# Kernel optimization log

Hardware: AMD Instinct MI355X
Metric: run time of the kernel (lower is better)

Reference implementation:

```python
import jax, jax.numpy as jnp
import numpy as np

B, T, D = 1, 4096, 2048
H = 16
D_NOPE, D_ROPE, D_V = 128, 64, 128
D_QK = D_NOPE + D_ROPE          # 192
KV_RANK = 512
SCALE = D_QK ** -0.5
EPS = 1e-5
ROPE_BASE = 10000.0


def _rope_tables(T, d):
    inv_freq = 1.0 / (ROPE_BASE ** (jnp.arange(0, d, 2, dtype=jnp.float32) / d))
    ang = jnp.arange(T, dtype=jnp.float32)[:, None] * inv_freq[None, :]  # [T, d/2]
    return jnp.cos(ang), jnp.sin(ang)


def _apply_rope(x, cos, sin):
    # x: [..., d]; cos/sin broadcastable to [..., d/2]; interleaved pairs
    x1, x2 = x[..., 0::2], x[..., 1::2]
    out = jnp.stack([x1 * cos - x2 * sin, x1 * sin + x2 * cos], axis=-1)
    return out.reshape(x.shape)


def _layernorm(x, g, b):
    mu = jnp.mean(x, axis=-1, keepdims=True)
    var = jnp.var(x, axis=-1, keepdims=True)
    return (x - mu) * jax.lax.rsqrt(var + EPS) * g + b


def setup_inputs() -> dict:
    key = jax.random.key(0)
    ks = jax.random.split(key, 6)
    s = 0.02
    return {
        "x": jax.random.normal(ks[0], (B, T, D), jnp.float32),
        "wq": jax.random.normal(ks[1], (H * D_QK, D), jnp.float32) * s,
        "wkv_a": jax.random.normal(ks[2], (KV_RANK + D_ROPE, D), jnp.float32) * s,
        "kv_gamma": jnp.ones((KV_RANK,), jnp.float32),
        "kv_beta": jnp.zeros((KV_RANK,), jnp.float32),
        "wkv_b": jax.random.normal(ks[3], (H * (D_NOPE + D_V), KV_RANK), jnp.float32) * s,
        "wo": jax.random.normal(ks[4], (D, H * D_V), jnp.float32) * s,
    }


def reference(x, wq, wkv_a, kv_gamma, kv_beta, wkv_b, wo):
    # Query projection (q_lora_rank == 0 path): [B,T,H,D_QK]
    q = (x @ wq.T).reshape(B, T, H, D_QK)
    q_nope, q_pe = q[..., :D_NOPE], q[..., D_NOPE:]

    # Low-rank KV projection: kv latent [B,T,KV_RANK], shared rope key [B,T,D_ROPE]
    kv_full = x @ wkv_a.T
    kv, k_pe = kv_full[..., :KV_RANK], kv_full[..., KV_RANK:]

    cos, sin = _rope_tables(T, D_ROPE)  # [T, D_ROPE/2]
    q_pe = _apply_rope(q_pe, cos[None, :, None, :], sin[None, :, None, :])
    k_pe = _apply_rope(k_pe, cos[None, :, :], sin[None, :, :])

    # Up-project normalized latent to per-head nope-keys and values
    kv = _layernorm(kv, kv_gamma, kv_beta)
    kvb = (kv @ wkv_b.T).reshape(B, T, H, D_NOPE + D_V)
    k_nope, v = kvb[..., :D_NOPE], kvb[..., D_NOPE:]

    # Scores: nope part per head + rope part with shared k_pe
    scores = (
        jnp.einsum("bshd,bthd->bhst", q_nope, k_nope)
        + jnp.einsum("bshd,btd->bhst", q_pe, k_pe)
    ) * SCALE

    causal = jnp.tril(jnp.ones((T, T), bool))
    scores = jnp.where(causal[None, None], scores, -jnp.inf)
    probs = jax.nn.softmax(scores, axis=-1)

    out = jnp.einsum("bhst,bthd->bshd", probs, v).reshape(B, T, H * D_V)
    return out @ wo.T
```

## Files before the change

### kernel.cpp

```cpp
#include <hip/hip_runtime.h>
#include <hip/hip_bf16.h>

typedef __attribute__((ext_vector_type(8))) short bf16x8;
typedef __attribute__((ext_vector_type(4))) float f32x4;
typedef __attribute__((address_space(3))) unsigned int lds_u32;
typedef __attribute__((address_space(1))) const unsigned int glb_u32;

#define LOG2_10000 13.287712379549449f
#define QSCALE (0.07216878364870323f * 1.4426950408889634f)

static __device__ __forceinline__ unsigned short f2bf(float f) {
  union { float f; unsigned int u; } v; v.f = f;
  unsigned int r = v.u + 0x7FFFu + ((v.u >> 16) & 1u);
  return (unsigned short)(r >> 16);
}
static __device__ __forceinline__ float bf2f(unsigned short h) {
  union { unsigned int u; float f; } v; v.u = ((unsigned int)h) << 16;
  return v.f;
}
static __device__ __forceinline__ f32x4 mfma16(bf16x8 a, bf16x8 b, f32x4 c) {
  return __builtin_amdgcn_mfma_f32_16x16x32_bf16(a, b, c, 0, 0, 0);
}
static __device__ __forceinline__ void gl_lds16(const void* g, void* l) {
  __builtin_amdgcn_global_load_lds((glb_u32*)g, (lds_u32*)l, 16, 0, 0);
}

__global__ __launch_bounds__(256) void cast_bf16(const float* __restrict__ src,
                                                 unsigned short* __restrict__ dst,
                                                 int nsrc, int ndst) {
  int i = (blockIdx.x * 256 + threadIdx.x) * 4;
  if (i >= ndst) return;
  float4 v = make_float4(0.f, 0.f, 0.f, 0.f);
  if (i < nsrc) v = *(const float4*)(src + i);
  uint2 o;
  o.x = (unsigned int)f2bf(v.x) | ((unsigned int)f2bf(v.y) << 16);
  o.y = (unsigned int)f2bf(v.z) | ((unsigned int)f2bf(v.w) << 16);
  *(uint2*)(dst + i) = o;
}

template <bool OUTBF>
__global__ __launch_bounds__(256, 2) void gemm_bf16(const unsigned short* __restrict__ A,
                                                    const unsigned short* __restrict__ Bt,
                                                    void* __restrict__ Cv,
                                                    int M, int N, int K, float alpha) {
  __shared__ unsigned short As[128 * 32];
  __shared__ unsigned short Bs[128 * 32];
  const int tid = threadIdx.x;
  const int w = tid >> 6, lane = tid & 63;
  const int quad = lane >> 4, l15 = lane & 15;
  const int wx = w & 1, wy = w >> 1;
  const int bm = blockIdx.y * 128, bn = blockIdx.x * 128;

  f32x4 acc[4][4];
#pragma unroll
  for (int i = 0; i < 4; ++i)
#pragma unroll
    for (int j = 0; j < 4; ++j) { acc[i][j][0] = 0.f; acc[i][j][1] = 0.f; acc[i][j][2] = 0.f; acc[i][j][3] = 0.f; }

  const int lrow = lane >> 2;
  const int lcol = (lane & 3) * 8;
  const unsigned short* Ag = A + (size_t)(bm + w * 16 + lrow) * K + lcol;
  const unsigned short* Bg = Bt + (size_t)(bn + w * 16 + lrow) * K + lcol;
  unsigned short* AsB = &As[(w * 16) * 32];
  unsigned short* BsB = &Bs[(w * 16) * 32];

  for (int k0 = 0; k0 < K; k0 += 32) {
    __syncthreads();
    gl_lds16(Ag + k0, AsB);
    gl_lds16(Ag + (size_t)64 * K + k0, AsB + 64 * 32);
    gl_lds16(Bg + k0, BsB);
    gl_lds16(Bg + (size_t)64 * K + k0, BsB + 64 * 32);
    __syncthreads();
    bf16x8 aF[4], bF[4];
#pragma unroll
    for (int i = 0; i < 4; ++i)
      aF[i] = *(const bf16x8*)&As[(wy * 64 + i * 16 + l15) * 32 + quad * 8];
#pragma unroll
    for (int j = 0; j < 4; ++j)
      bF[j] = *(const bf16x8*)&Bs[(wx * 64 + j * 16 + l15) * 32 + quad * 8];
#pragma unroll
    for (int i = 0; i < 4; ++i)
#pragma unroll
      for (int j = 0; j < 4; ++j)
        acc[i][j] = mfma16(aF[i], bF[j], acc[i][j]);
  }

#pragma unroll
  for (int i = 0; i < 4; ++i)
#pragma unroll
    for (int r = 0; r < 4; ++r) {
      const size_t row = (size_t)(bm + wy * 64 + i * 16 + quad * 4 + r) * (size_t)N;
#pragma unroll
      for (int j = 0; j < 4; ++j) {
        const int col = bn + wx * 64 + j * 16 + l15;
        if (OUTBF) ((unsigned short*)Cv)[row + col] = f2bf(acc[i][j][r] * alpha);
        else       ((float*)Cv)[row + col] = acc[i][j][r];
      }
    }
}

__global__ __launch_bounds__(256) void rope_q_bf(unsigned short* __restrict__ qh) {
  int idx = blockIdx.x * 256 + threadIdx.x;
  int j = idx & 31;
  int th = idx >> 5;
  int h = th & 15;
  int t = th >> 4;
  float fr = exp2f(-(float)j * (LOG2_10000 / 32.f));
  float ang = (float)t * fr;
  float sn, cs;
  sincosf(ang, &sn, &cs);
  unsigned short* p = qh + (size_t)t * 3072 + h * 192 + 128 + 2 * j;
  unsigned int v = *(unsigned int*)p;
  float a = bf2f((unsigned short)v), b = bf2f((unsigned short)(v >> 16));
  float na = a * cs - b * sn, nb = a * sn + b * cs;
  *(unsigned int*)p = (unsigned int)f2bf(na) | ((unsigned int)f2bf(nb) << 16);
}

__global__ __launch_bounds__(256) void ln_rope_k(const float* __restrict__ kvfull,
                                                 const float* __restrict__ gamma,
                                                 const float* __restrict__ beta,
                                                 unsigned short* __restrict__ kvln,
                                                 unsigned short* __restrict__ kpe) {
  const int t = blockIdx.x;
  const int tid = threadIdx.x;
  const float* row = kvfull + (size_t)t * 640;
  float x0 = row[tid], x1 = row[tid + 256];
  float sm = x0 + x1;
  float sq = x0 * x0 + x1 * x1;
#pragma unroll
  for (int off = 1; off < 64; off <<= 1) {
    sm += __shfl_xor(sm, off, 64);
    sq += __shfl_xor(sq, off, 64);
  }
  __shared__ float rs[4], rq[4];
  const int lane = tid & 63, wid = tid >> 6;
  if (lane == 0) { rs[wid] = sm; rq[wid] = sq; }
  __syncthreads();
  float tsm = rs[0] + rs[1] + rs[2] + rs[3];
  float tsq = rq[0] + rq[1] + rq[2] + rq[3];
  float mu = tsm * (1.f / 512.f);
  float var = tsq * (1.f / 512.f) - mu * mu;
  float inv = rsqrtf(var + 1e-5f);
  kvln[(size_t)t * 512 + tid]       = f2bf((x0 - mu) * inv * gamma[tid] + beta[tid]);
  kvln[(size_t)t * 512 + tid + 256] = f2bf((x1 - mu) * inv * gamma[tid + 256] + beta[tid + 256]);
  if (tid < 32) {
    float a = row[512 + 2 * tid], b = row[512 + 2 * tid + 1];
    float fr = exp2f(-(float)tid * (LOG2_10000 / 32.f));
    float ang = (float)t * fr;
    float sn, cs;
    sincosf(ang, &sn, &cs);
    kpe[(size_t)t * 64 + 2 * tid]     = f2bf(a * cs - b * sn);
    kpe[(size_t)t * 64 + 2 * tid + 1] = f2bf(a * sn + b * cs);
  }
}

__global__ __launch_bounds__(256) void transpose_v(const unsigned short* __restrict__ kvb,
                                                   unsigned short* __restrict__ Vt) {
  __shared__ unsigned short tile[64][72];
  const int tb = blockIdx.x * 64;
  const int h  = blockIdx.y >> 1;
  const int c0 = (blockIdx.y & 1) * 64;
  const int tid = threadIdx.x;
  const int r  = tid >> 4;
  const int c4 = (tid & 15) * 4;
#pragma unroll
  for (int rep = 0; rep < 4; ++rep) {
    const int t = rep * 16 + r;
    uint2 d = *(const uint2*)(kvb + (size_t)(tb + t) * 4096 + h * 256 + 128 + c0 + c4);
    *(uint2*)&tile[t][c4] = d;
  }
  __syncthreads();
#pragma unroll
  for (int rep = 0; rep < 4; ++rep) {
    const int c = rep * 16 + r;
    unsigned int lo = (unsigned int)tile[c4 + 0][c] | ((unsigned int)tile[c4 + 1][c] << 16);
    unsigned int hi = (unsigned int)tile[c4 + 2][c] | ((unsigned int)tile[c4 + 3][c] << 16);
    uint2 o; o.x = lo; o.y = hi;
    *(uint2*)(Vt + ((size_t)h * 128 + c0 + c) * 4096 + tb + c4) = o;
  }
}

__global__ __launch_bounds__(256, 2) void attn_mfma(const unsigned short* __restrict__ qh,
                                                    const unsigned short* __restrict__ kvb,
                                                    const unsigned short* __restrict__ kpe,
                                                    const unsigned short* __restrict__ Vt,
                                                    unsigned short* __restrict__ attnh) {
  __shared__ unsigned short sK[6 * 2048];
  __shared__ unsigned short sVt[128 * 64];
  __shared__ unsigned short sP[128 * 72];

  const int bid = blockIdx.x;
  const int h = bid & 15;
  const int z = bid >> 4;
  const int qt = (z < 16) ? (31 - z) : (z - 16);
  const int q0 = qt * 128;
  const int tid = threadIdx.x;
  const int w = tid >> 6, lane = tid & 63;
  const int quad = lane >> 4, l15 = lane & 15;
  const int wq0 = w * 32;

  const unsigned short* kvbh = kvb + h * 256;
  const unsigned short* Vth = Vt + (size_t)h * 128 * 4096;

  bf16x8 qF[2][6];
#pragma unroll
  for (int i = 0; i < 2; ++i)
#pragma unroll
    for (int g = 0; g < 6; ++g) {
      const int grow = q0 + wq0 + i * 16 + l15;
      union { uint4 u; bf16x8 v; } tmp;
      tmp.u = *(const uint4*)(qh + (size_t)grow * 3072 + h * 192 + g * 32 + quad * 8);
      qF[i][g] = tmp.v;
    }

  f32x4 oA[2][8];
  float mi[2], li[2];
#pragma unroll
  for (int i = 0; i < 2; ++i) {
    mi[i] = -1e30f; li[i] = 0.f;
#pragma unroll
    for (int j = 0; j < 8; ++j) { oA[i][j][0] = 0.f; oA[i][j][1] = 0.f; oA[i][j][2] = 0.f; oA[i][j][3] = 0.f; }
  }

  const int nk = 2 * (qt + 1);
  for (int kt = 0; kt < nk; ++kt) {
    const int k0 = kt * 64;
    __syncthreads();

#pragma unroll
    for (int j = 0; j < 6; ++j) {
      const int i = w * 6 + j;
      const int granule = i * 64 + lane;
      const int g = granule >> 8;
      const int key = (granule >> 2) & 63;
      const int col = (g << 5) + ((granule & 3) << 3);
      const unsigned short* src = (col < 128)
          ? kvbh + (size_t)(k0 + key) * 4096 + col
          : kpe + (size_t)(k0 + key) * 64 + (col - 128);
      gl_lds16(src, &sK[i * 512]);
    }
#pragma unroll
    for (int j = 0; j < 4; ++j) {
      const int ii = w * 4 + j;
      const int n = ii * 8 + (lane >> 3);
      const int b = (lane & 7) ^ ((lane >> 3) & 7);
      gl_lds16(Vth + (size_t)n * 4096 + k0 + b * 8, &sVt[ii * 512]);
    }
    __syncthreads();

    f32x4 sc[4][2];
#pragma unroll
    for (int kk = 0; kk < 4; ++kk)
#pragma unroll
      for (int i = 0; i < 2; ++i) { sc[kk][i][0] = 0.f; sc[kk][i][1] = 0.f; sc[kk][i][2] = 0.f; sc[kk][i][3] = 0.f; }
#pragma unroll
    for (int g = 0; g < 6; ++g) {
      bf16x8 kF[4];
#pragma unroll
      for (int kk = 0; kk < 4; ++kk)
        kF[kk] = *(const bf16x8*)&sK[g * 2048 + (kk * 16 + l15) * 32 + quad * 8];
#pragma unroll
      for (int kk = 0; kk < 4; ++kk)
#pragma unroll
        for (int i = 0; i < 2; ++i)
          sc[kk][i] = mfma16(kF[kk], qF[i][g], sc[kk][i]);
    }

    const bool msk = (kt >= 2 * qt);
    float alpha[2];
#pragma unroll
    for (int i = 0; i < 2; ++i) {
      const int grow = q0 + wq0 + i * 16 + l15;
      if (msk) {
#pragma unroll
        for (int kk = 0; kk < 4; ++kk)
#pragma unroll
          for (int rr = 0; rr < 4; ++rr) {
            const int gk = k0 + kk * 16 + quad * 4 + rr;
            if (gk > grow) sc[kk][i][rr] = -1e30f;
          }
      }
      float mx = -1e30f;
#pragma unroll
      for (int kk = 0; kk < 4; ++kk)
#pragma unroll
        for (int rr = 0; rr < 4; ++rr) mx = fmaxf(mx, sc[kk][i][rr]);
      mx = fmaxf(mx, __shfl_xor(mx, 16, 64));
      mx = fmaxf(mx, __shfl_xor(mx, 32, 64));
      const float mnew = fmaxf(mi[i], mx);
      alpha[i] = __builtin_amdgcn_exp2f(mi[i] - mnew);
      float sum = 0.f;
#pragma unroll
      for (int kk = 0; kk < 4; ++kk)
#pragma unroll
        for (int rr = 0; rr < 4; ++rr) {
          const float p = __builtin_amdgcn_exp2f(sc[kk][i][rr] - mnew);
          sc[kk][i][rr] = p;
          sum += p;
        }
      sum += __shfl_xor(sum, 16, 64);
      sum += __shfl_xor(sum, 32, 64);
      li[i] = li[i] * alpha[i] + sum;
      mi[i] = mnew;
    }

#pragma unroll
    for (int i = 0; i < 2; ++i)
#pragma unroll
      for (int rr = 0; rr < 4; ++rr) {
        const float af = __shfl(alpha[i], (lane & 48) | (quad * 4 + rr), 64);
#pragma unroll
        for (int j = 0; j < 8; ++j) oA[i][j][rr] *= af;
      }

#pragma unroll
    for (int kk = 0; kk < 4; ++kk)
#pragma unroll
      for (int i = 0; i < 2; ++i) {
        union { float f; unsigned int u; } p0, p1, p2, p3;
        p0.f = sc[kk][i][0]; p1.f = sc[kk][i][1]; p2.f = sc[kk][i][2]; p3.f = sc[kk][i][3];
        uint2 pk;
        pk.x = (p0.u >> 16) | (p1.u & 0xFFFF0000u);
        pk.y = (p2.u >> 16) | (p3.u & 0xFFFF0000u);
        *(uint2*)&sP[(size_t)(wq0 + i * 16 + l15) * 72 + kk * 16 + quad * 4] = pk;
      }

#pragma unroll
    for (int ks = 0; ks < 2; ++ks) {
      bf16x8 pF[2], vF[8];
#pragma unroll
      for (int i = 0; i < 2; ++i)
        pF[i] = *(const bf16x8*)&sP[(size_t)(wq0 + i * 16 + l15) * 72 + ks * 32 + quad * 8];
#pragma unroll
      for (int j = 0; j < 8; ++j) {
        const int n = j * 16 + l15;
        const int blk = (ks * 4 + quad) ^ (l15 & 7);
        vF[j] = *(const bf16x8*)&sVt[(size_t)n * 64 + blk * 8];
      }
#pragma unroll
      for (int i = 0; i < 2; ++i)
#pragma unroll
        for (int j = 0; j < 8; ++j)
          oA[i][j] = mfma16(pF[i], vF[j], oA[i][j]);
    }
  }

  float linv[2];
  linv[0] = 1.f / li[0];
  linv[1] = 1.f / li[1];
#pragma unroll
  for (int i = 0; i < 2; ++i)
#pragma unroll
    for (int rr = 0; rr < 4; ++rr) {
      const float lf = __shfl(linv[i], (lane & 48) | (quad * 4 + rr), 64);
      const size_t grow = (size_t)(q0 + wq0 + i * 16 + quad * 4 + rr);
#pragma unroll
      for (int j = 0; j < 8; ++j)
        attnh[grow * 2048 + h * 128 + j * 16 + l15] = f2bf(oA[i][j][rr] * lf);
    }
}

extern "C" void kernel_launch(void* const* d_in, const int* in_sizes, int n_in,
                              void* d_out, int out_size, void* d_ws, size_t ws_size,
                              hipStream_t stream) {
  const float* x        = (const float*)d_in[0];
  const float* wq       = (const float*)d_in[1];
  const float* wkv_a    = (const float*)d_in[2];
  const float* kv_gamma = (const float*)d_in[3];
  const float* kv_beta  = (const float*)d_in[4];
  const float* wkv_b    = (const float*)d_in[5];
  const float* wo       = (const float*)d_in[6];
  float* out = (float*)d_out;

  char* p = (char*)d_ws;
  unsigned short* xh    = (unsigned short*)p; p += (size_t)4096 * 2048 * 2;
  unsigned short* wqh   = (unsigned short*)p; p += (size_t)3072 * 2048 * 2;
  unsigned short* wah   = (unsigned short*)p; p += (size_t)640 * 2048 * 2;
  unsigned short* wbh   = (unsigned short*)p; p += (size_t)4096 * 512 * 2;
  unsigned short* woh   = (unsigned short*)p; p += (size_t)2048 * 2048 * 2;
  unsigned short* qh    = (unsigned short*)p; p += (size_t)4096 * 3072 * 2;
  float*          kvful = (float*)p;          p += (size_t)4096 * 640 * 4;
  unsigned short* kvlnh = (unsigned short*)p; p += (size_t)4096 * 512 * 2;
  unsigned short* kpeh  = (unsigned short*)p; p += (size_t)4096 * 64 * 2;
  unsigned short* kvbh  = (unsigned short*)p; p += (size_t)4096 * 4096 * 2;
  unsigned short* attnh = (unsigned short*)p; p += (size_t)4096 * 2048 * 2;
  if ((size_t)(p - (char*)d_ws) > ws_size) return;
  unsigned short* Vt = xh;

  cast_bf16<<<8192, 256, 0, stream>>>(x,     xh,  4096 * 2048, 4096 * 2048);
  cast_bf16<<<6144, 256, 0, stream>>>(wq,    wqh, 3072 * 2048, 3072 * 2048);
  cast_bf16<<<1280, 256, 0, stream>>>(wkv_a, wah, 576 * 2048,  640 * 2048);
  cast_bf16<<<2048, 256, 0, stream>>>(wkv_b, wbh, 4096 * 512,  4096 * 512);
  cast_bf16<<<4096, 256, 0, stream>>>(wo,    woh, 2048 * 2048, 2048 * 2048);

  gemm_bf16<true><<<dim3(24, 32), 256, 0, stream>>>(xh, wqh, qh, 4096, 3072, 2048, QSCALE);
  rope_q_bf<<<8192, 256, 0, stream>>>(qh);
  gemm_bf16<false><<<dim3(5, 32), 256, 0, stream>>>(xh, wah, kvful, 4096, 640, 2048, 1.f);
  ln_rope_k<<<4096, 256, 0, stream>>>(kvful, kv_gamma, kv_beta, kvlnh, kpeh);
  gemm_bf16<true><<<dim3(32, 32), 256, 0, stream>>>(kvlnh, wbh, kvbh, 4096, 4096, 512, 1.f);
  transpose_v<<<dim3(64, 32), 256, 0, stream>>>(kvbh, Vt);
  attn_mfma<<<512, 256, 0, stream>>>(qh, kvbh, kpeh, Vt, attnh);
  gemm_bf16<false><<<dim3(16, 32), 256, 0, stream>>>(attnh, woh, out, 4096, 2048, 2048, 1.f);
}
```

Before: 490.5 us.

## Split attention work across 8 waves with 16 query rows each

The attention kernel now launches 512 threads per block, so 8 waves each own 16 query rows instead of 4 waves owning 32. This shrinks per-wave register state (Q fragments, accumulators, scores) to raise occupancy and latency hiding, and splits the K/V tile loads across more waves. In exchange, each K and V fragment read from LDS feeds half as many MFMAs, which raises LDS read traffic per FLOP and adds more waves to every barrier.

```diff
diff --git a/kernel.cpp b/kernel.cpp
--- a/kernel.cpp
+++ b/kernel.cpp
@@ -180,7 +180,7 @@
   }
 }
 
-__global__ __launch_bounds__(256, 2) void attn_mfma(const unsigned short* __restrict__ qh,
+__global__ __launch_bounds__(512, 4) void attn_mfma(const unsigned short* __restrict__ qh,
                                                     const unsigned short* __restrict__ kvb,
                                                     const unsigned short* __restrict__ kpe,
                                                     const unsigned short* __restrict__ Vt,
@@ -197,30 +197,24 @@
   const int tid = threadIdx.x;
   const int w = tid >> 6, lane = tid & 63;
   const int quad = lane >> 4, l15 = lane & 15;
-  const int wq0 = w * 32;
+  const int wq0 = w * 16;
 
   const unsigned short* kvbh = kvb + h * 256;
   const unsigned short* Vth = Vt + (size_t)h * 128 * 4096;
 
-  bf16x8 qF[2][6];
-#pragma unroll
-  for (int i = 0; i < 2; ++i)
-#pragma unroll
-    for (int g = 0; g < 6; ++g) {
-      const int grow = q0 + wq0 + i * 16 + l15;
-      union { uint4 u; bf16x8 v; } tmp;
-      tmp.u = *(const uint4*)(qh + (size_t)grow * 3072 + h * 192 + g * 32 + quad * 8);
-      qF[i][g] = tmp.v;
-    }
-
-  f32x4 oA[2][8];
-  float mi[2], li[2];
-#pragma unroll
-  for (int i = 0; i < 2; ++i) {
-    mi[i] = -1e30f; li[i] = 0.f;
-#pragma unroll
-    for (int j = 0; j < 8; ++j) { oA[i][j][0] = 0.f; oA[i][j][1] = 0.f; oA[i][j][2] = 0.f; oA[i][j][3] = 0.f; }
-  }
+  bf16x8 qF[6];
+#pragma unroll
+  for (int g = 0; g < 6; ++g) {
+    const int grow = q0 + wq0 + l15;
+    union { uint4 u; bf16x8 v; } tmp;
+    tmp.u = *(const uint4*)(qh + (size_t)grow * 3072 + h * 192 + g * 32 + quad * 8);
+    qF[g] = tmp.v;
+  }
+
+  f32x4 oA[8];
+  float mi = -1e30f, li = 0.f;
+#pragma unroll
+  for (int j = 0; j < 8; ++j) { oA[j][0] = 0.f; oA[j][1] = 0.f; oA[j][2] = 0.f; oA[j][3] = 0.f; }
 
   const int nk = 2 * (qt + 1);
   for (int kt = 0; kt < nk; ++kt) {
@@ -228,8 +222,8 @@
     __syncthreads();
 
 #pragma unroll
-    for (int j = 0; j < 6; ++j) {
-      const int i = w * 6 + j;
+    for (int j = 0; j < 3; ++j) {
+      const int i = w * 3 + j;
       const int granule = i * 64 + lane;
       const int g = granule >> 8;
       const int key = (granule >> 2) & 63;
@@ -240,19 +234,17 @@
       gl_lds16(src, &sK[i * 512]);
     }
 #pragma unroll
-    for (int j = 0; j < 4; ++j) {
-      const int ii = w * 4 + j;
+    for (int j = 0; j < 2; ++j) {
+      const int ii = w * 2 + j;
       const int n = ii * 8 + (lane >> 3);
       const int b = (lane & 7) ^ ((lane >> 3) & 7);
       gl_lds16(Vth + (size_t)n * 4096 + k0 + b * 8, &sVt[ii * 512]);
     }
     __syncthreads();
 
-    f32x4 sc[4][2];
-#pragma unroll
-    for (int kk = 0; kk < 4; ++kk)
-#pragma unroll
-      for (int i = 0; i < 2; ++i) { sc[kk][i][0] = 0.f; sc[kk][i][1] = 0.f; sc[kk][i][2] = 0.f; sc[kk][i][3] = 0.f; }
+    f32x4 sc[4];
+#pragma unroll
+    for (int kk = 0; kk < 4; ++kk) { sc[kk][0] = 0.f; sc[kk][1] = 0.f; sc[kk][2] = 0.f; sc[kk][3] = 0.f; }
 #pragma unroll
     for (int g = 0; g < 6; ++g) {
       bf16x8 kF[4];
@@ -261,76 +253,67 @@
         kF[kk] = *(const bf16x8*)&sK[g * 2048 + (kk * 16 + l15) * 32 + quad * 8];
 #pragma unroll
       for (int kk = 0; kk < 4; ++kk)
-#pragma unroll
-        for (int i = 0; i < 2; ++i)
-          sc[kk][i] = mfma16(kF[kk], qF[i][g], sc[kk][i]);
+        sc[kk] = mfma16(kF[kk], qF[g], sc[kk]);
     }
 
     const bool msk = (kt >= 2 * qt);
-    float alpha[2];
-#pragma unroll
-    for (int i = 0; i < 2; ++i) {
-      const int grow = q0 + wq0 + i * 16 + l15;
+    float alpha;
+    {
+      const int grow = q0 + wq0 + l15;
       if (msk) {
 #pragma unroll
         for (int kk = 0; kk < 4; ++kk)
 #pragma unroll
           for (int rr = 0; rr < 4; ++rr) {
             const int gk = k0 + kk * 16 + quad * 4 + rr;
-            if (gk > grow) sc[kk][i][rr] = -1e30f;
+            if (gk > grow) sc[kk][rr] = -1e30f;
           }
       }
       float mx = -1e30f;
 #pragma unroll
       for (int kk = 0; kk < 4; ++kk)
 #pragma unroll
-        for (int rr = 0; rr < 4; ++rr) mx = fmaxf(mx, sc[kk][i][rr]);
+        for (int rr = 0; rr < 4; ++rr) mx = fmaxf(mx, sc[kk][rr]);
       mx = fmaxf(mx, __shfl_xor(mx, 16, 64));
       mx = fmaxf(mx, __shfl_xor(mx, 32, 64));
-      const float mnew = fmaxf(mi[i], mx);
-      alpha[i] = __builtin_amdgcn_exp2f(mi[i] - mnew);
+      const float mnew = fmaxf(mi, mx);
+      alpha = __builtin_amdgcn_exp2f(mi - mnew);
       float sum = 0.f;
 #pragma unroll
       for (int kk = 0; kk < 4; ++kk)
 #pragma unroll
         for (int rr = 0; rr < 4; ++rr) {
-          const float p = __builtin_amdgcn_exp2f(sc[kk][i][rr] - mnew);
-          sc[kk][i][rr] = p;
+          const float p = __builtin_amdgcn_exp2f(sc[kk][rr] - mnew);
+          sc[kk][rr] = p;
           sum += p;
         }
       sum += __shfl_xor(sum, 16, 64);
       sum += __shfl_xor(sum, 32, 64);
-      li[i] = li[i] * alpha[i] + sum;
-      mi[i] = mnew;
-    }
-
-#pragma unroll
-    for (int i = 0; i < 2; ++i)
-#pragma unroll
-      for (int rr = 0; rr < 4; ++rr) {
-        const float af = __shfl(alpha[i], (lane & 48) | (quad * 4 + rr), 64);
-#pragma unroll
-        for (int j = 0; j < 8; ++j) oA[i][j][rr] *= af;
-      }
-
-#pragma unroll
-    for (int kk = 0; kk < 4; ++kk)
-#pragma unroll
-      for (int i = 0; i < 2; ++i) {
-        union { float f; unsigned int u; } p0, p1, p2, p3;
-        p0.f = sc[kk][i][0]; p1.f = sc[kk][i][1]; p2.f = sc[kk][i][2]; p3.f = sc[kk][i][3];
-        uint2 pk;
-        pk.x = (p0.u >> 16) | (p1.u & 0xFFFF0000u);
-        pk.y = (p2.u >> 16) | (p3.u & 0xFFFF0000u);
-        *(uint2*)&sP[(size_t)(wq0 + i * 16 + l15) * 72 + kk * 16 + quad * 4] = pk;
-      }
+      li = li * alpha + sum;
+      mi = mnew;
+    }
+
+#pragma unroll
+    for (int rr = 0; rr < 4; ++rr) {
+      const float af = __shfl(alpha, (lane & 48) | (quad * 4 + rr), 64);
+#pragma unroll
+      for (int j = 0; j < 8; ++j) oA[j][rr] *= af;
+    }
+
+#pragma unroll
+    for (int kk = 0; kk < 4; ++kk) {
+      union { float f; unsigned int u; } p0, p1, p2, p3;
+      p0.f = sc[kk][0]; p1.f = sc[kk][1]; p2.f = sc[kk][2]; p3.f = sc[kk][3];
+      uint2 pk;
+      pk.x = (p0.u >> 16) | (p1.u & 0xFFFF0000u);
+      pk.y = (p2.u >> 16) | (p3.u & 0xFFFF0000u);
+      *(uint2*)&sP[(size_t)(wq0 + l15) * 72 + kk * 16 + quad * 4] = pk;
+    }
 
 #pragma unroll
     for (int ks = 0; ks < 2; ++ks) {
-      bf16x8 pF[2], vF[8];
-#pragma unroll
-      for (int i = 0; i < 2; ++i)
-        pF[i] = *(const bf16x8*)&sP[(size_t)(wq0 + i * 16 + l15) * 72 + ks * 32 + quad * 8];
+      bf16x8 pF, vF[8];
+      pF = *(const bf16x8*)&sP[(size_t)(wq0 + l15) * 72 + ks * 32 + quad * 8];
 #pragma unroll
       for (int j = 0; j < 8; ++j) {
         const int n = j * 16 + l15;
@@ -338,26 +321,20 @@
         vF[j] = *(const bf16x8*)&sVt[(size_t)n * 64 + blk * 8];
       }
 #pragma unroll
-      for (int i = 0; i < 2; ++i)
-#pragma unroll
-        for (int j = 0; j < 8; ++j)
-          oA[i][j] = mfma16(pF[i], vF[j], oA[i][j]);
-    }
-  }
-
-  float linv[2];
-  linv[0] = 1.f / li[0];
-  linv[1] = 1.f / li[1];
-#pragma unroll
-  for (int i = 0; i < 2; ++i)
-#pragma unroll
-    for (int rr = 0; rr < 4; ++rr) {
-      const float lf = __shfl(linv[i], (lane & 48) | (quad * 4 + rr), 64);
-      const size_t grow = (size_t)(q0 + wq0 + i * 16 + quad * 4 + rr);
-#pragma unroll
       for (int j = 0; j < 8; ++j)
-        attnh[grow * 2048 + h * 128 + j * 16 + l15] = f2bf(oA[i][j][rr] * lf);
-    }
+        oA[j] = mfma16(pF, vF[j], oA[j]);
+    }
+  }
+
+  const float linv = 1.f / li;
+#pragma unroll
+  for (int rr = 0; rr < 4; ++rr) {
+    const float lf = __shfl(linv, (lane & 48) | (quad * 4 + rr), 64);
+    const size_t grow = (size_t)(q0 + wq0 + quad * 4 + rr);
+#pragma unroll
+    for (int j = 0; j < 8; ++j)
+      attnh[grow * 2048 + h * 128 + j * 16 + l15] = f2bf(oA[j][rr] * lf);
+  }
 }
 
 extern "C" void kernel_launch(void* const* d_in, const int* in_sizes, int n_in,
@@ -399,6 +376,6 @@
   ln_rope_k<<<4096, 256, 0, stream>>>(kvful, kv_gamma, kv_beta, kvlnh, kpeh);
   gemm_bf16<true><<<dim3(32, 32), 256, 0, stream>>>(kvlnh, wbh, kvbh, 4096, 4096, 512, 1.f);
   transpose_v<<<dim3(64, 32), 256, 0, stream>>>(kvbh, Vt);
-  attn_mfma<<<512, 256, 0, stream>>>(qh, kvbh, kpeh, Vt, attnh);
+  attn_mfma<<<512, 512, 0, stream>>>(qh, kvbh, kpeh, Vt, attnh);
   gemm_bf16<false><<<dim3(16, 32), 256, 0, stream>>>(attnh, woh, out, 4096, 2048, 2048, 1.f);
 }
```

New measurement: 508.0 us. 1.04x slower.

## Double-buffer K tiles in LDS and load V directly into registers

Applied to the files above, without the earlier changes.

The K tile (nope+rope) is now double-buffered in LDS, so the next tile is prefetched via global_load_lds while the current one is consumed. Manual s_waitcnt vmcnt counts plus raw s_barrier replace __syncthreads. V fragments are no longer staged through LDS. Each wave loads its 16 V fragments straight from global memory into registers at the start of the iteration, which frees LDS but adds register pressure and uncoalesced-ish global loads. The hand-tuned vmcnt values depend on the exact instruction counts and are fragile; an LDS barrier is added after QK before the P writes.

```diff
diff --git a/kernel.cpp b/kernel.cpp
--- a/kernel.cpp
+++ b/kernel.cpp
@@ -180,13 +180,30 @@
   }
 }
 
+static __device__ __forceinline__ void stage_k(const unsigned short* kvbh,
+                                               const unsigned short* kpe,
+                                               int k0, unsigned short* dst,
+                                               int w, int lane) {
+#pragma unroll
+  for (int j = 0; j < 6; ++j) {
+    const int i = w * 6 + j;
+    const int granule = i * 64 + lane;
+    const int g = granule >> 8;
+    const int key = (granule >> 2) & 63;
+    const int col = (g << 5) + ((granule & 3) << 3);
+    const unsigned short* src = (col < 128)
+        ? kvbh + (size_t)(k0 + key) * 4096 + col
+        : kpe + (size_t)(k0 + key) * 64 + (col - 128);
+    gl_lds16(src, dst + i * 512);
+  }
+}
+
 __global__ __launch_bounds__(256, 2) void attn_mfma(const unsigned short* __restrict__ qh,
                                                     const unsigned short* __restrict__ kvb,
                                                     const unsigned short* __restrict__ kpe,
                                                     const unsigned short* __restrict__ Vt,
                                                     unsigned short* __restrict__ attnh) {
-  __shared__ unsigned short sK[6 * 2048];
-  __shared__ unsigned short sVt[128 * 64];
+  __shared__ unsigned short sK[2][6 * 2048];
   __shared__ unsigned short sP[128 * 72];
 
   const int bid = blockIdx.x;
@@ -223,31 +240,33 @@
   }
 
   const int nk = 2 * (qt + 1);
+
+  stage_k(kvbh, kpe, 0, &sK[0][0], w, lane);
+
   for (int kt = 0; kt < nk; ++kt) {
     const int k0 = kt * 64;
-    __syncthreads();
-
-#pragma unroll
-    for (int j = 0; j < 6; ++j) {
-      const int i = w * 6 + j;
-      const int granule = i * 64 + lane;
-      const int g = granule >> 8;
-      const int key = (granule >> 2) & 63;
-      const int col = (g << 5) + ((granule & 3) << 3);
-      const unsigned short* src = (col < 128)
-          ? kvbh + (size_t)(k0 + key) * 4096 + col
-          : kpe + (size_t)(k0 + key) * 64 + (col - 128);
-      gl_lds16(src, &sK[i * 512]);
-    }
-#pragma unroll
-    for (int j = 0; j < 4; ++j) {
-      const int ii = w * 4 + j;
-      const int n = ii * 8 + (lane >> 3);
-      const int b = (lane & 7) ^ ((lane >> 3) & 7);
-      gl_lds16(Vth + (size_t)n * 4096 + k0 + b * 8, &sVt[ii * 512]);
-    }
-    __syncthreads();
-
+    const int p = kt & 1;
+
+    if (kt + 1 < nk)
+      stage_k(kvbh, kpe, k0 + 64, &sK[p ^ 1][0], w, lane);
+    __asm__ __volatile__("" ::: "memory");
+
+    bf16x8 vr[2][8];
+#pragma unroll
+    for (int ks = 0; ks < 2; ++ks)
+#pragma unroll
+      for (int j = 0; j < 8; ++j) {
+        union { uint4 u; bf16x8 v; } t;
+        t.u = *(const uint4*)(Vth + (size_t)(j * 16 + l15) * 4096 + k0 + ks * 32 + quad * 8);
+        vr[ks][j] = t.v;
+      }
+
+    if (kt + 1 < nk) { __asm__ __volatile__("s_waitcnt vmcnt(22)" ::: "memory"); }
+    else             { __asm__ __volatile__("s_waitcnt vmcnt(16)" ::: "memory"); }
+    __builtin_amdgcn_s_barrier();
+    __asm__ __volatile__("" ::: "memory");
+
+    const unsigned short* sKp = &sK[p][0];
     f32x4 sc[4][2];
 #pragma unroll
     for (int kk = 0; kk < 4; ++kk)
@@ -258,13 +277,17 @@
       bf16x8 kF[4];
 #pragma unroll
       for (int kk = 0; kk < 4; ++kk)
-        kF[kk] = *(const bf16x8*)&sK[g * 2048 + (kk * 16 + l15) * 32 + quad * 8];
+        kF[kk] = *(const bf16x8*)&sKp[g * 2048 + (kk * 16 + l15) * 32 + quad * 8];
 #pragma unroll
       for (int kk = 0; kk < 4; ++kk)
 #pragma unroll
         for (int i = 0; i < 2; ++i)
           sc[kk][i] = mfma16(kF[kk], qF[i][g], sc[kk][i]);
     }
+
+    __asm__ __volatile__("s_waitcnt lgkmcnt(0)" ::: "memory");
+    __builtin_amdgcn_s_barrier();
+    __asm__ __volatile__("" ::: "memory");
 
     const bool msk = (kt >= 2 * qt);
     float alpha[2];
@@ -294,9 +317,9 @@
       for (int kk = 0; kk < 4; ++kk)
 #pragma unroll
         for (int rr = 0; rr < 4; ++rr) {
-          const float p = __builtin_amdgcn_exp2f(sc[kk][i][rr] - mnew);
-          sc[kk][i][rr] = p;
-          sum += p;
+          const float pe = __builtin_amdgcn_exp2f(sc[kk][i][rr] - mnew);
+          sc[kk][i][rr] = pe;
+          sum += pe;
         }
       sum += __shfl_xor(sum, 16, 64);
       sum += __shfl_xor(sum, 32, 64);
@@ -327,21 +350,15 @@
 
 #pragma unroll
     for (int ks = 0; ks < 2; ++ks) {
-      bf16x8 pF[2], vF[8];
+      bf16x8 pF[2];
 #pragma unroll
       for (int i = 0; i < 2; ++i)
         pF[i] = *(const bf16x8*)&sP[(size_t)(wq0 + i * 16 + l15) * 72 + ks * 32 + quad * 8];
 #pragma unroll
-      for (int j = 0; j < 8; ++j) {
-        const int n = j * 16 + l15;
-        const int blk = (ks * 4 + quad) ^ (l15 & 7);
-        vF[j] = *(const bf16x8*)&sVt[(size_t)n * 64 + blk * 8];
-      }
-#pragma unroll
       for (int i = 0; i < 2; ++i)
 #pragma unroll
         for (int j = 0; j < 8; ++j)
-          oA[i][j] = mfma16(pF[i], vF[j], oA[i][j]);
+          oA[i][j] = mfma16(pF[i], vr[ks][j], oA[i][j]);
     }
   }
 
```

Result: slower. 751.2 us (+53.2%).
